# Kernel tuning notes

Measured on AMD Instinct MI355X. Metric: run time of the kernel, lower is better.

Reference implementation:

```python
import jax, jax.numpy as jnp
import numpy as np

IN_F, OUT_F, GS = 4096, 16384, 128


def setup_inputs() -> dict:
    key = jax.random.key(0)
    k1, k2, k3 = jax.random.split(key, 3)
    x = jax.random.normal(k1, (2, 1024, IN_F), dtype=jnp.float32)
    # ternary codes in {-1, 0, 1}, stored as int8 in the original module
    ternary = jax.random.randint(k2, (OUT_F, IN_F), -1, 2, dtype=jnp.int32)
    n_groups = OUT_F * IN_F // GS
    # per-group scales: positive, like beta = mean(|w|) per group
    scales = jax.random.uniform(k3, (n_groups,), dtype=jnp.float32, minval=0.01, maxval=0.1)
    return {"x": x, "ternary": ternary, "scales": scales}


def reference(x, ternary, scales):
    # Dequantize: each contiguous group of GS flattened weight entries shares one scale.
    w = (ternary.astype(jnp.float32).reshape(-1, GS) * scales[:, None]).reshape(OUT_F, IN_F)
    # F.linear(x, w) == x @ w.T
    return jnp.einsum('bsi,oi->bso', x, w)
```

## Files before the change

### kernel.cpp

```cpp
#include <hip/hip_runtime.h>
#include <hip/hip_bf16.h>
#include <stdint.h>

#define M_ROWS 2048
#define IN_F   4096
#define OUT_F  16384

#define BM 128
#define BN 128
#define BK 64

typedef __attribute__((ext_vector_type(8))) short short8;
typedef __attribute__((ext_vector_type(4))) float floatx4;

__device__ __forceinline__ unsigned short f32_to_bf16_rne(float f) {
    union { float f; uint32_t u; } v; v.f = f;
    uint32_t u = v.u;
    return (unsigned short)((u + 0x7FFFu + ((u >> 16) & 1u)) >> 16);
}

__global__ __launch_bounds__(256) void convert_x_kernel(
        const float* __restrict__ x, unsigned short* __restrict__ xb) {
    int t = blockIdx.x * 256 + threadIdx.x;
    const float4* p = (const float4*)(x + (size_t)t * 8);
    float4 a = p[0];
    float4 b = p[1];
    short8 o;
    o[0] = (short)f32_to_bf16_rne(a.x);
    o[1] = (short)f32_to_bf16_rne(a.y);
    o[2] = (short)f32_to_bf16_rne(a.z);
    o[3] = (short)f32_to_bf16_rne(a.w);
    o[4] = (short)f32_to_bf16_rne(b.x);
    o[5] = (short)f32_to_bf16_rne(b.y);
    o[6] = (short)f32_to_bf16_rne(b.z);
    o[7] = (short)f32_to_bf16_rne(b.w);
    *(short8*)(xb + (size_t)t * 8) = o;
}

__device__ __forceinline__ unsigned int pack2(int t0, int t1, float s) {
    float w0 = (float)t0 * s;
    float w1 = (float)t1 * s;
    return __builtin_amdgcn_perm(__float_as_uint(w1), __float_as_uint(w0),
                                 0x07060302u);
}

__global__ __launch_bounds__(256, 3) void gemm_fused_kernel(
        const unsigned short* __restrict__ A,
        const int* __restrict__ T,
        const float* __restrict__ S,
        float* __restrict__ C) {
    __shared__ unsigned short As[BM * BK];
    __shared__ unsigned short Bs[BN * BK];

    const int tid  = threadIdx.x;
    const int lane = tid & 63;
    const int quad = lane >> 4;
    const int frow = lane & 15;
    const int r7   = frow & 7;
    const int w    = tid >> 6;
    const int wm   = (w & 1) * 64;
    const int wn   = (w >> 1) * 64;

    const int bm = blockIdx.x * BM;
    const int bn = blockIdx.y * BN;

    const int r0   = tid >> 3;
    const int jcol = (tid & 7) ^ (r0 & 7);

    floatx4 acc[4][4] = {};

    int a_off[2][4], b_off[2][4];
#pragma unroll
    for (int ks = 0; ks < 2; ++ks) {
        const int j = ks * 4 + quad;
        const int sw = (j ^ r7) * 8;
#pragma unroll
        for (int t2 = 0; t2 < 4; ++t2) {
            a_off[ks][t2] = (wm + t2 * 16 + frow) * BK + sw;
            b_off[ks][t2] = (wn + t2 * 16 + frow) * BK + sw;
        }
    }

    for (int kt = 0; kt < IN_F; kt += BK) {
        __syncthreads();

        int4 q0[4], q1[4];
        float sc[4];
#pragma unroll
        for (int i = 0; i < 4; ++i) {
            const int row = r0 + 32 * i;
            const int* gp = T + (size_t)(bn + row) * IN_F + kt + jcol * 8;
            q0[i] = *(const int4*)gp;
            q1[i] = *(const int4*)(gp + 4);
            sc[i] = S[(size_t)(bn + row) * 32 + (kt >> 7)];
        }

#pragma unroll
        for (int i = 0; i < 4; ++i) {
            const int c    = 256 * i + tid;
            const int crow = c >> 3;
            const int jg   = (c & 7) ^ (crow & 7);
            const int ub   = (256 * i + (tid & 192)) * 8;
            const unsigned short* ga =
                A + (size_t)(bm + crow) * IN_F + kt + jg * 8;
            __builtin_amdgcn_global_load_lds(
                (const __attribute__((address_space(1))) void*)ga,
                (__attribute__((address_space(3))) void*)(As + ub), 16, 0, 0);
        }

#pragma unroll
        for (int i = 0; i < 4; ++i) {
            const float s = __uint_as_float(__float_as_uint(sc[i]) + 0x8000u);
            int4 o;
            o.x = (int)pack2(q0[i].x, q0[i].y, s);
            o.y = (int)pack2(q0[i].z, q0[i].w, s);
            o.z = (int)pack2(q1[i].x, q1[i].y, s);
            o.w = (int)pack2(q1[i].z, q1[i].w, s);
            *(int4*)(Bs + (size_t)(256 * i + tid) * 8) = o;
        }

        __syncthreads();

#pragma unroll
        for (int ks = 0; ks < 2; ++ks) {
            short8 af[4], bf[4];
#pragma unroll
            for (int t2 = 0; t2 < 4; ++t2) {
                af[t2] = *(const short8*)(As + a_off[ks][t2]);
                bf[t2] = *(const short8*)(Bs + b_off[ks][t2]);
            }
#pragma unroll
            for (int mt = 0; mt < 4; ++mt)
#pragma unroll
                for (int nt = 0; nt < 4; ++nt)
                    acc[mt][nt] = __builtin_amdgcn_mfma_f32_16x16x32_bf16(
                        af[mt], bf[nt], acc[mt][nt], 0, 0, 0);
        }
    }

    const int row0 = bm + wm + quad * 4;
    const int col0 = bn + wn + frow;
#pragma unroll
    for (int mt = 0; mt < 4; ++mt) {
#pragma unroll
        for (int nt = 0; nt < 4; ++nt) {
            float* cp = C + (size_t)(row0 + mt * 16) * OUT_F + (col0 + nt * 16);
#pragma unroll
            for (int r = 0; r < 4; ++r)
                cp[(size_t)r * OUT_F] = acc[mt][nt][r];
        }
    }
}

extern "C" void kernel_launch(void* const* d_in, const int* in_sizes, int n_in,
                              void* d_out, int out_size, void* d_ws, size_t ws_size,
                              hipStream_t stream) {
    const float* x    = (const float*)d_in[0];
    const int*   tern = (const int*)d_in[1];
    const float* scal = (const float*)d_in[2];
    float*       out  = (float*)d_out;

    unsigned short* xb = (unsigned short*)d_ws;

    convert_x_kernel<<<(M_ROWS * IN_F / 8) / 256, 256, 0, stream>>>(x, xb);
    gemm_fused_kernel<<<dim3(M_ROWS / BM, OUT_F / BN), 256, 0, stream>>>(
        xb, tern, scal, out);
}
```

Measured before the change: 788.7 us.

## Pack ternary weights to 2-bit codes in a pre-pass and dequantize bitwise

```diff
diff --git a/kernel.cpp b/kernel.cpp
--- a/kernel.cpp
+++ b/kernel.cpp
@@ -13,10 +13,10 @@
 typedef __attribute__((ext_vector_type(8))) short short8;
 typedef __attribute__((ext_vector_type(4))) float floatx4;
 
-__device__ __forceinline__ unsigned short f32_to_bf16_rne(float f) {
+__device__ __forceinline__ unsigned int f32_to_bf16_rne(float f) {
     union { float f; uint32_t u; } v; v.f = f;
     uint32_t u = v.u;
-    return (unsigned short)((u + 0x7FFFu + ((u >> 16) & 1u)) >> 16);
+    return (u + 0x7FFFu + ((u >> 16) & 1u)) >> 16;
 }
 
 __global__ __launch_bounds__(256) void convert_x_kernel(
@@ -37,16 +37,35 @@
     *(short8*)(xb + (size_t)t * 8) = o;
 }
 
-__device__ __forceinline__ unsigned int pack2(int t0, int t1, float s) {
-    float w0 = (float)t0 * s;
-    float w1 = (float)t1 * s;
-    return __builtin_amdgcn_perm(__float_as_uint(w1), __float_as_uint(w0),
-                                 0x07060302u);
+__device__ __forceinline__ unsigned int code2(int t) {
+    return (unsigned int)((t & 1) | ((t >> 30) & 2));
+}
+__global__ __launch_bounds__(256) void pack_t_kernel(
+        const int* __restrict__ tern, unsigned int* __restrict__ tp) {
+    int g = blockIdx.x * 256 + threadIdx.x;
+    const int4* p = (const int4*)(tern + (size_t)g * 16);
+    unsigned int c = 0;
+#pragma unroll
+    for (int q = 0; q < 4; ++q) {
+        int4 v = p[q];
+        c |= code2(v.x) << (8 * q + 0);
+        c |= code2(v.y) << (8 * q + 2);
+        c |= code2(v.z) << (8 * q + 4);
+        c |= code2(v.w) << (8 * q + 6);
+    }
+    tp[g] = c;
+}
+
+__device__ __forceinline__ unsigned int dq2(unsigned int b4, unsigned int sbb) {
+    unsigned int b = b4 & 0xFu;
+    unsigned int p = (b | (b << 14)) & 0x10001u;
+    unsigned int m = p * 0xFFFFu;
+    return (m & sbb) | ((b & 2u) << 14) | ((b & 8u) << 28);
 }
 
 __global__ __launch_bounds__(256, 3) void gemm_fused_kernel(
         const unsigned short* __restrict__ A,
-        const int* __restrict__ T,
+        const unsigned short* __restrict__ T2,
         const float* __restrict__ S,
         float* __restrict__ C) {
     __shared__ unsigned short As[BM * BK];
@@ -81,18 +100,24 @@
         }
     }
 
+    unsigned int sbb[4];
+
     for (int kt = 0; kt < IN_F; kt += BK) {
         __syncthreads();
 
-        int4 q0[4], q1[4];
-        float sc[4];
+        unsigned int cw[4];
 #pragma unroll
         for (int i = 0; i < 4; ++i) {
-            const int row = r0 + 32 * i;
-            const int* gp = T + (size_t)(bn + row) * IN_F + kt + jcol * 8;
-            q0[i] = *(const int4*)gp;
-            q1[i] = *(const int4*)(gp + 4);
-            sc[i] = S[(size_t)(bn + row) * 32 + (kt >> 7)];
+            const int row = bn + r0 + 32 * i;
+            cw[i] = T2[(size_t)row * (IN_F / 8) + (kt >> 3) + jcol];
+        }
+        if ((kt & 127) == 0) {
+#pragma unroll
+            for (int i = 0; i < 4; ++i) {
+                const int row = bn + r0 + 32 * i;
+                const float s = S[(size_t)row * (IN_F / 128) + (kt >> 7)];
+                sbb[i] = f32_to_bf16_rne(s) * 0x10001u;
+            }
         }
 
 #pragma unroll
@@ -110,12 +135,12 @@
 
 #pragma unroll
         for (int i = 0; i < 4; ++i) {
-            const float s = __uint_as_float(__float_as_uint(sc[i]) + 0x8000u);
+            const unsigned int c = cw[i], sb2 = sbb[i];
             int4 o;
-            o.x = (int)pack2(q0[i].x, q0[i].y, s);
-            o.y = (int)pack2(q0[i].z, q0[i].w, s);
-            o.z = (int)pack2(q1[i].x, q1[i].y, s);
-            o.w = (int)pack2(q1[i].z, q1[i].w, s);
+            o.x = (int)dq2(c,       sb2);
+            o.y = (int)dq2(c >> 4,  sb2);
+            o.z = (int)dq2(c >> 8,  sb2);
+            o.w = (int)dq2(c >> 12, sb2);
             *(int4*)(Bs + (size_t)(256 * i + tid) * 8) = o;
         }
 
@@ -161,8 +186,10 @@
     float*       out  = (float*)d_out;
 
     unsigned short* xb = (unsigned short*)d_ws;
+    unsigned int*   tp = (unsigned int*)(xb + (size_t)M_ROWS * IN_F);
 
     convert_x_kernel<<<(M_ROWS * IN_F / 8) / 256, 256, 0, stream>>>(x, xb);
+    pack_t_kernel<<<((size_t)OUT_F * IN_F / 16) / 256, 256, 0, stream>>>(tern, tp);
     gemm_fused_kernel<<<dim3(M_ROWS / BM, OUT_F / BN), 256, 0, stream>>>(
-        xb, tern, scal, out);
+        xb, (const unsigned short*)tp, scal, out);
 }
```

New measurement: 728.5 us. -7.6%, faster.
